# Performance work log

Hardware: AMD Instinct MI355X
Metric: run time of the kernel (lower is better)

Reference implementation:

```python
import jax, jax.numpy as jnp
from jax import lax
import numpy as np

DIM = 256
RANK = 128
E = 4      # num_experts
K = 2      # top_k
B, H, W = 8, 128, 128


def setup_inputs() -> dict:
    key = jax.random.key(0)
    ks = jax.random.split(key, 12)
    s = lambda fan: 1.0 / np.sqrt(fan)
    return {
        "x": jax.random.normal(ks[0], (B, DIM, H, W), jnp.float32),
        "shared": jax.random.normal(ks[1], (B, DIM, H, W), jnp.float32),
        # FrequencyEmbedding MLP (torch Linear: weight [out,in], bias [out])
        "mlp_w1": jax.random.normal(ks[2], (2 * DIM, DIM), jnp.float32) * s(DIM),
        "mlp_b1": jnp.zeros((2 * DIM,), jnp.float32),
        "mlp_w2": jax.random.normal(ks[3], (DIM, 2 * DIM), jnp.float32) * s(2 * DIM),
        "mlp_b2": jnp.zeros((DIM,), jnp.float32),
        # routing gates (no bias)
        "gate_w": jax.random.normal(ks[4], (E, DIM), jnp.float32) * s(DIM),
        "freq_gate_w": jax.random.normal(ks[5], (E, DIM), jnp.float32) * s(DIM),
        # stacked expert 1x1 convs: proj0/proj1 dim->rank, proj2 rank->dim
        "p0": jax.random.normal(ks[6], (E, RANK, DIM), jnp.float32) * s(DIM),
        "p1": jax.random.normal(ks[7], (E, RANK, DIM), jnp.float32) * s(DIM),
        "p2": jax.random.normal(ks[8], (E, DIM, RANK), jnp.float32) * s(RANK),
        # output 1x1 conv (no bias)
        "proj_out_w": jax.random.normal(ks[9], (DIM, DIM), jnp.float32) * s(DIM),
    }


def _high_pass_depthwise(x):
    # fixed frozen 3x3 high-pass kernel, depthwise (groups=C)
    C = x.shape[1]
    k = jnp.array([[-1., -1., -1.], [-1., 8., -1.], [-1., -1., -1.]], x.dtype)
    k = jnp.tile(k[None, None], (C, 1, 1, 1))  # [C,1,3,3]
    return lax.conv_general_dilated(
        x, k, window_strides=(1, 1), padding="SAME",
        feature_group_count=C,
        dimension_numbers=("NCHW", "OIHW", "NCHW"))


def reference(x, shared, mlp_w1, mlp_b1, mlp_w2, mlp_b2,
              gate_w, freq_gate_w, p0, p1, p2, proj_out_w):
    Bn = x.shape[0]
    # FrequencyEmbedding: high-pass conv -> GELU -> global mean -> MLP
    h = jax.nn.gelu(_high_pass_depthwise(x), approximate=False)
    h = h.mean(axis=(-2, -1))                                    # [B, C]
    freq_emb = jax.nn.gelu(h @ mlp_w1.T + mlp_b1, approximate=False) @ mlp_w2.T + mlp_b2
    # Routing: avg-pool gate + freq gate, softmax, top-k, scatter to dense gates
    pooled = x.mean(axis=(-2, -1))                               # [B, C]
    logits = pooled @ gate_w.T + freq_emb @ freq_gate_w.T        # [B, E]
    gating = jax.nn.softmax(logits, axis=-1)
    vals, idx = lax.top_k(gating, K)                             # [B, K]
    gates = jnp.zeros_like(logits).at[jnp.arange(Bn)[:, None], idx].set(vals)  # [B, E]
    a = jnp.einsum("erd,bdhw->berhw", p0, x)                     # [B,E,R,H,W]
    b = jnp.einsum("erd,bdhw->berhw", p1, shared)
    y = a * jax.nn.silu(b)
    # gate-weighted combine, folding gates into the contraction; shortcut term
    combined = (jnp.einsum("be,edr,berhw->bdhw", gates, p2, y)
                + gates.sum(-1)[:, None, None, None] * x)        # [B,C,H,W]
    out = jnp.einsum("od,bdhw->bohw", proj_out_w, combined)
    return out
```

## Files before the change

kernel.cpp:

```cpp
#include <hip/hip_runtime.h>
#include <math.h>

#define DIMC 256
#define HW   16384
#define NB   8
#define HID  512
#define NE   4
#define RNK  128

typedef __bf16 bf16x8 __attribute__((ext_vector_type(8)));
typedef float  f32x4  __attribute__((ext_vector_type(4)));
typedef float  f32x16 __attribute__((ext_vector_type(16)));

__device__ __forceinline__ unsigned short f2bf(float f) {
  unsigned u = __builtin_bit_cast(unsigned, f);
  u += 0x7FFFu + ((u >> 16) & 1u);
  return (unsigned short)(u >> 16);
}
__device__ __forceinline__ unsigned pack2(float a, float b) {
  return (unsigned)f2bf(a) | ((unsigned)f2bf(b) << 16);
}
__device__ __forceinline__ float bf2f(unsigned short u) {
  unsigned v = ((unsigned)u) << 16;
  return __builtin_bit_cast(float, v);
}

#define CPAD 136
__global__ __launch_bounds__(256) void k_conv_reduce(const float* __restrict__ x,
                                                     float* __restrict__ xsum,
                                                     float* __restrict__ hsum) {
  __shared__ unsigned short sp[128 * CPAD];
  __shared__ float red[8];
  const int p = blockIdx.x;
  const int tid = threadIdx.x;
  const float4* img4 = (const float4*)(x + (size_t)p * HW);
#pragma unroll
  for (int u = 0; u < 16; ++u) {
    const int unit = tid + 256 * u;
    const float4 v = img4[unit];
    const int row = unit >> 5, xq = unit & 31;
    uint2 w;
    w.x = pack2(v.x, v.y);
    w.y = pack2(v.z, v.w);
    *(uint2*)&sp[row * CPAD + xq * 4] = w;
  }
  __syncthreads();

  float xacc = 0.f, hacc = 0.f;
#pragma unroll
  for (int u = 0; u < 4; ++u) {
    const int seg = tid + 256 * u;
    const int row = seg >> 3, x0 = (seg & 7) * 16;
    float S[16], c[16];
#pragma unroll
    for (int j = 0; j < 16; ++j) S[j] = 0.f;
#pragma unroll
    for (int dr = -1; dr <= 1; ++dr) {
      const int r2 = row + dr;
      float v[18];
      if ((unsigned)r2 <= 127u) {
        const unsigned short* rp = sp + r2 * CPAD + x0;
        const uint4 q0 = *(const uint4*)(rp);
        const uint4 q1 = *(const uint4*)(rp + 8);
        v[0]  = (x0 > 0)        ? bf2f(rp[-1]) : 0.f;
        v[17] = (x0 + 16 < 128) ? bf2f(rp[16]) : 0.f;
        v[1] = bf2f((unsigned short)(q0.x & 0xffff)); v[2] = bf2f((unsigned short)(q0.x >> 16));
        v[3] = bf2f((unsigned short)(q0.y & 0xffff)); v[4] = bf2f((unsigned short)(q0.y >> 16));
        v[5] = bf2f((unsigned short)(q0.z & 0xffff)); v[6] = bf2f((unsigned short)(q0.z >> 16));
        v[7] = bf2f((unsigned short)(q0.w & 0xffff)); v[8] = bf2f((unsigned short)(q0.w >> 16));
        v[9]  = bf2f((unsigned short)(q1.x & 0xffff)); v[10] = bf2f((unsigned short)(q1.x >> 16));
        v[11] = bf2f((unsigned short)(q1.y & 0xffff)); v[12] = bf2f((unsigned short)(q1.y >> 16));
        v[13] = bf2f((unsigned short)(q1.z & 0xffff)); v[14] = bf2f((unsigned short)(q1.z >> 16));
        v[15] = bf2f((unsigned short)(q1.w & 0xffff)); v[16] = bf2f((unsigned short)(q1.w >> 16));
      } else {
#pragma unroll
        for (int j = 0; j < 18; ++j) v[j] = 0.f;
      }
      if (dr == 0) {
#pragma unroll
        for (int j = 0; j < 16; ++j) c[j] = v[j + 1];
      }
#pragma unroll
      for (int j = 0; j < 16; ++j) S[j] += v[j] + v[j + 1] + v[j + 2];
    }
#pragma unroll
    for (int j = 0; j < 16; ++j) {
      const float h = 9.f * c[j] - S[j];
      hacc += 0.5f * h * (1.f + erff(h * 0.70710678118654752f));
      xacc += c[j];
    }
  }
#pragma unroll
  for (int off = 32; off > 0; off >>= 1) {
    xacc += __shfl_down(xacc, off);
    hacc += __shfl_down(hacc, off);
  }
  const int wid = tid >> 6, lane = tid & 63;
  if (lane == 0) { red[wid] = xacc; red[4 + wid] = hacc; }
  __syncthreads();
  if (tid == 0) {
    xsum[p] = red[0] + red[1] + red[2] + red[3];
    hsum[p] = red[4] + red[5] + red[6] + red[7];
  }
}

__global__ __launch_bounds__(256) void k_gate_t1(
    const float* __restrict__ hsum, const float* __restrict__ w1,
    const float* __restrict__ b1, float* __restrict__ t1) {
  const int blk = blockIdx.x;
  const int b = blk >> 7;
  const int o = (blk & 127) * 4 + (threadIdx.x >> 6);
  const int lane = threadIdx.x & 63;
  const float4 h = *(const float4*)(hsum + b * DIMC + lane * 4);
  const float4 w = *(const float4*)(w1 + (size_t)o * DIMC + lane * 4);
  float acc = h.x * w.x + h.y * w.y + h.z * w.z + h.w * w.w;
#pragma unroll
  for (int off = 32; off > 0; off >>= 1) acc += __shfl_down(acc, off);
  if (lane == 0) {
    acc = acc * (1.f / 16384.f) + b1[o];
    t1[b * HID + o] = 0.5f * acc * (1.f + erff(acc * 0.70710678118654752f));
  }
}

__global__ __launch_bounds__(256) void k_gate_fe(
    const float* __restrict__ t1, const float* __restrict__ w2,
    const float* __restrict__ b2, float* __restrict__ fe) {
  const int blk = blockIdx.x;
  const int b = blk >> 6;
  const int o = (blk & 63) * 4 + (threadIdx.x >> 6);
  const int lane = threadIdx.x & 63;
  const float* tr = t1 + b * HID + lane * 8;
  const float* wr = w2 + (size_t)o * HID + lane * 8;
  const float4 ta = *(const float4*)tr,  tb = *(const float4*)(tr + 4);
  const float4 wa = *(const float4*)wr,  wb = *(const float4*)(wr + 4);
  float acc = ta.x * wa.x + ta.y * wa.y + ta.z * wa.z + ta.w * wa.w
            + tb.x * wb.x + tb.y * wb.y + tb.z * wb.z + tb.w * wb.w;
#pragma unroll
  for (int off = 32; off > 0; off >>= 1) acc += __shfl_down(acc, off);
  if (lane == 0) fe[b * DIMC + o] = acc + b2[o];
}

__global__ __launch_bounds__(256) void k_gate_fin(
    const float* __restrict__ xsum, const float* __restrict__ fe,
    const float* __restrict__ gw, const float* __restrict__ fgw,
    float* __restrict__ gates, float* __restrict__ gsumv, int* __restrict__ sel) {
  __shared__ float slog[NB][NE];
  const int wave = threadIdx.x >> 6, lane = threadIdx.x & 63;
  const int e = wave;
  const float4 g1 = *(const float4*)(gw + e * DIMC + lane * 4);
  const float4 g2 = *(const float4*)(fgw + e * DIMC + lane * 4);
  for (int b = 0; b < NB; ++b) {
    const float4 p = *(const float4*)(xsum + b * DIMC + lane * 4);
    const float4 f = *(const float4*)(fe + b * DIMC + lane * 4);
    float acc = (p.x * g1.x + p.y * g1.y + p.z * g1.z + p.w * g1.w) * (1.f / 16384.f)
              + f.x * g2.x + f.y * g2.y + f.z * g2.z + f.w * g2.w;
#pragma unroll
    for (int off = 32; off > 0; off >>= 1) acc += __shfl_down(acc, off);
    if (lane == 0) slog[b][e] = acc;
  }
  __syncthreads();
  if (threadIdx.x < NB) {
    const int b = threadIdx.x;
    float l[4] = {slog[b][0], slog[b][1], slog[b][2], slog[b][3]};
    const float m = fmaxf(fmaxf(l[0], l[1]), fmaxf(l[2], l[3]));
    float g[4];
    float ssum = 0.f;
    for (int e2 = 0; e2 < 4; ++e2) { g[e2] = expf(l[e2] - m); ssum += g[e2]; }
    for (int e2 = 0; e2 < 4; ++e2) g[e2] /= ssum;
    int i1 = 0;
    for (int e2 = 1; e2 < 4; ++e2) if (g[e2] > g[i1]) i1 = e2;
    int i2 = -1;
    for (int e2 = 0; e2 < 4; ++e2) {
      if (e2 == i1) continue;
      if (i2 < 0 || g[e2] > g[i2]) i2 = e2;
    }
    for (int e2 = 0; e2 < 4; ++e2)
      gates[b * 4 + e2] = (e2 == i1) ? g[i1] : ((e2 == i2) ? g[i2] : 0.f);
    gsumv[b] = g[i1] + g[i2];
    sel[b * 2 + 0] = i1;
    sel[b * 2 + 1] = i2;
  }
}

__global__ __launch_bounds__(128) void k_q2(const float* __restrict__ wp,
                                            const float* __restrict__ p2,
                                            float* __restrict__ q2) {
  const int eo = blockIdx.x;
  const int e = eo >> 8, o = eo & 255;
  const int r = threadIdx.x;
  const float* p2e = p2 + (size_t)e * DIMC * RNK;
  const float* wrow = wp + (size_t)o * DIMC;
  float acc = 0.f;
  for (int d = 0; d < DIMC; ++d) acc += wrow[d] * p2e[d * RNK + r];
  q2[(size_t)eo * RNK + r] = acc;
}

__global__ __launch_bounds__(256) void k_build(
    const float* __restrict__ p0, const float* __restrict__ p1,
    const float* __restrict__ wp, const float* __restrict__ q2,
    const float* __restrict__ gates, const float* __restrict__ gsumv,
    const int* __restrict__ sel,
    unsigned* __restrict__ A1u, unsigned* __restrict__ A2u,
    unsigned* __restrict__ A3u) {
  const int total = NB * 32768;
  for (int id = blockIdx.x * 256 + threadIdx.x; id < total;
       id += gridDim.x * 256) {
    const int b = id >> 15;
    const int gi = id & 32767;
    uint4 wv;
    unsigned* dst;
    if (gi < 16384) {
      const int t = gi >> 13;
      const int gj = gi & 8191;
      const int rowblk = gj >> 10, ks = (gj >> 6) & 15;
      const int h = (gj >> 5) & 1, r = gj & 31;
      const int row = rowblk * 32 + r;
      const int e = sel[b * 2 + (row >> 7)];
      const float* src = (t ? p1 : p0) + ((size_t)e * 128 + (row & 127)) * 256
                       + ks * 16 + h * 8;
      const float4 v0 = *(const float4*)src;
      const float4 v1 = *(const float4*)(src + 4);
      wv.x = pack2(v0.x, v0.y); wv.y = pack2(v0.z, v0.w);
      wv.z = pack2(v1.x, v1.y); wv.w = pack2(v1.z, v1.w);
      dst = (t ? A2u : A1u) + (size_t)b * 32768 + gj * 4;
    } else {
      const int gj = gi - 16384;
      const int rowblk = gj >> 11, ks = (gj >> 6) & 31;
      const int h = (gj >> 5) & 1, r = gj & 31;
      const int o = rowblk * 32 + r;
      const int k = ks * 16 + h * 8;
      float v[8];
      if (k < 256) {
        const int e = sel[b * 2 + (k >> 7)];
        const float gsc = gates[b * 4 + e];
        const float* qq = q2 + ((size_t)e * 256 + o) * RNK + (k & 127);
#pragma unroll
        for (int j = 0; j < 8; ++j) v[j] = gsc * qq[j];
      } else {
        const float gs = gsumv[b];
        const float* wr = wp + (size_t)o * DIMC + (k - 256);
#pragma unroll
        for (int j = 0; j < 8; ++j) v[j] = gs * wr[j];
      }
      wv.x = pack2(v[0], v[1]); wv.y = pack2(v[2], v[3]);
      wv.z = pack2(v[4], v[5]); wv.w = pack2(v[6], v[7]);
      dst = A3u + (size_t)b * 65536 + gj * 4;
    }
    *(uint4*)dst = wv;
  }
}

__global__ __launch_bounds__(512, 4) void k_main_mfma(
    const float* __restrict__ x, const float* __restrict__ shr,
    const unsigned short* __restrict__ A1b, const unsigned short* __restrict__ A2b,
    const unsigned short* __restrict__ A3b, float* __restrict__ out) {
  __shared__ unsigned short XF[16384];
  __shared__ unsigned short SF[16384];
  const int tid = threadIdx.x;
  const int b = blockIdx.x & 7;
  const int tile = blockIdx.x >> 3;
  const int nb0 = tile * 64;
  const int wave = tid >> 6;
  const int lane = tid & 63;
  const int r32 = lane & 31;
  const int h = lane >> 5;
  const int wrow = wave * 32;
  const size_t pbase = (size_t)b * DIMC * HW + nb0;

  {
    const int px = lane;
#pragma unroll
    for (int pass = 0; pass < 4; ++pass) {
      const int dblk = pass * 8 + wave;
      const float* xc = x   + pbase + (size_t)(dblk * 8) * HW + px;
      const float* sc = shr + pbase + (size_t)(dblk * 8) * HW + px;
      float vx[8], vs[8];
#pragma unroll
      for (int jj = 0; jj < 8; ++jj) {
        vx[jj] = xc[(size_t)jj * HW];
        vs[jj] = sc[(size_t)jj * HW];
      }
      const int o = dblk * 512 + ((px ^ (dblk & 7)) << 3);
      uint4 wv;
      wv.x = pack2(vx[0], vx[1]); wv.y = pack2(vx[2], vx[3]);
      wv.z = pack2(vx[4], vx[5]); wv.w = pack2(vx[6], vx[7]);
      *(uint4*)&XF[o] = wv;
      uint4 sv;
      sv.x = pack2(vs[0], vs[1]); sv.y = pack2(vs[2], vs[3]);
      sv.z = pack2(vs[4], vs[5]); sv.w = pack2(vs[6], vs[7]);
      *(uint4*)&SF[o] = sv;
    }
  }
  __syncthreads();

  const unsigned short* A1w = A1b + (size_t)(b * 8 + wave) * 8192;
  const unsigned short* A2w = A2b + (size_t)(b * 8 + wave) * 8192;
  const unsigned short* A3w = A3b + (size_t)(b * 8 + wave) * 16384;

  f32x16 accB0 = (f32x16)0.f, accB1 = (f32x16)0.f;
#pragma unroll
  for (int ks = 0; ks < 16; ++ks) {
    const bf16x8 a = *(const bf16x8*)(A2w + ks * 512 + lane * 8);
    const int dblkB = ks * 2 + h;
    const int eb = dblkB * 512 + ((r32 ^ (dblkB & 7)) << 3);
    const bf16x8 b0 = *(const bf16x8*)&SF[eb];
    const bf16x8 b1 = *(const bf16x8*)&SF[eb + 256];
    accB0 = __builtin_amdgcn_mfma_f32_32x32x16_bf16(a, b0, accB0, 0, 0, 0);
    accB1 = __builtin_amdgcn_mfma_f32_32x32x16_bf16(a, b1, accB1, 0, 0, 0);
  }

  f32x16 accA0 = (f32x16)0.f, accA1 = (f32x16)0.f;
#pragma unroll
  for (int ks = 0; ks < 16; ++ks) {
    const bf16x8 a1 = *(const bf16x8*)(A1w + ks * 512 + lane * 8);
    const int dblkB = ks * 2 + h;
    const int eb = dblkB * 512 + ((r32 ^ (dblkB & 7)) << 3);
    const bf16x8 b0 = *(const bf16x8*)&XF[eb];
    const bf16x8 b1 = *(const bf16x8*)&XF[eb + 256];
    accA0 = __builtin_amdgcn_mfma_f32_32x32x16_bf16(a1, b0, accA0, 0, 0, 0);
    accA1 = __builtin_amdgcn_mfma_f32_32x32x16_bf16(a1, b1, accA1, 0, 0, 0);
  }
  __syncthreads();

#pragma unroll
  for (int q = 0; q < 4; ++q) {
    const int dblk = wave * 4 + q;
    const int sw = dblk & 7;
    const int base = dblk * 512 + h * 4;
    float y0[4], y1[4];
#pragma unroll
    for (int i = 0; i < 4; ++i) {
      const float bA = accB0[q * 4 + i];
      const float bBv = accB1[q * 4 + i];
      y0[i] = accA0[q * 4 + i] * (bA / (1.f + __expf(-bA)));
      y1[i] = accA1[q * 4 + i] * (bBv / (1.f + __expf(-bBv)));
    }
    uint2 w0; w0.x = pack2(y0[0], y0[1]); w0.y = pack2(y0[2], y0[3]);
    *(uint2*)&SF[base + ((r32 ^ sw) << 3)] = w0;
    uint2 w1; w1.x = pack2(y1[0], y1[1]); w1.y = pack2(y1[2], y1[3]);
    *(uint2*)&SF[base + (((32 + r32) ^ sw) << 3)] = w1;
  }
  __syncthreads();

  f32x16 accO0 = (f32x16)0.f, accO1 = (f32x16)0.f;
#pragma unroll
  for (int ks = 0; ks < 32; ++ks) {
    const bf16x8 a3 = *(const bf16x8*)(A3w + ks * 512 + lane * 8);
    const int kk = ks & 15;
    const unsigned short* Bsrc = (ks < 16) ? SF : XF;
    const int dblkB = kk * 2 + h;
    const int eb = dblkB * 512 + ((r32 ^ (dblkB & 7)) << 3);
    const bf16x8 b0 = *(const bf16x8*)&Bsrc[eb];
    const bf16x8 b1 = *(const bf16x8*)&Bsrc[eb + 256];
    accO0 = __builtin_amdgcn_mfma_f32_32x32x16_bf16(a3, b0, accO0, 0, 0, 0);
    accO1 = __builtin_amdgcn_mfma_f32_32x32x16_bf16(a3, b1, accO1, 0, 0, 0);
  }

  {
    float* ob = out + pbase;
#pragma unroll
    for (int r = 0; r < 16; ++r) {
      const int row = wrow + (r & 3) + 8 * (r >> 2) + 4 * h;
      ob[(size_t)row * HW + r32] = accO0[r];
      ob[(size_t)row * HW + 32 + r32] = accO1[r];
    }
  }
}

extern "C" void kernel_launch(void* const* d_in, const int* in_sizes, int n_in,
                              void* d_out, int out_size, void* d_ws, size_t ws_size,
                              hipStream_t stream) {
  (void)in_sizes; (void)n_in; (void)out_size; (void)ws_size;
  const float* x   = (const float*)d_in[0];
  const float* shr = (const float*)d_in[1];
  const float* w1  = (const float*)d_in[2];
  const float* b1  = (const float*)d_in[3];
  const float* w2  = (const float*)d_in[4];
  const float* b2  = (const float*)d_in[5];
  const float* gw  = (const float*)d_in[6];
  const float* fgw = (const float*)d_in[7];
  const float* p0  = (const float*)d_in[8];
  const float* p1  = (const float*)d_in[9];
  const float* p2  = (const float*)d_in[10];
  const float* wp  = (const float*)d_in[11];
  float* out = (float*)d_out;

  float* ws    = (float*)d_ws;
  float* xsum  = ws;
  float* hsum  = ws + 2048;
  float* gates = ws + 4096;
  float* gsumv = ws + 4128;
  int*   sel   = (int*)(ws + 4136);
  float* q2    = ws + 4152;
  unsigned* A1u = (unsigned*)(ws + 135224);
  unsigned* A2u = A1u + NB * 256 * 128;
  unsigned* A3u = A2u + NB * 256 * 128;
  float* t1g   = (float*)(A3u + NB * 256 * 256);
  float* feg   = t1g + NB * HID;

  k_conv_reduce<<<NB * DIMC, 256, 0, stream>>>(x, xsum, hsum);
  k_gate_t1<<<1024, 256, 0, stream>>>(hsum, w1, b1, t1g);
  k_gate_fe<<<512, 256, 0, stream>>>(t1g, w2, b2, feg);
  k_gate_fin<<<1, 256, 0, stream>>>(xsum, feg, gw, fgw, gates, gsumv, sel);
  k_q2<<<NE * DIMC, 128, 0, stream>>>(wp, p2, q2);
  k_build<<<512, 256, 0, stream>>>(p0, p1, wp, q2, gates, gsumv, sel, A1u, A2u, A3u);
  k_main_mfma<<<2048, 512, 0, stream>>>(x, shr,
      (const unsigned short*)A1u, (const unsigned short*)A2u,
      (const unsigned short*)A3u, out);
}
```

Baseline: 264.4 us.

## Fuse gating MLP kernels into one per-batch kernel, retile q2, use native bf16 casts

Merges the three gating kernels (t1, freq embedding, final softmax/top-k) into one kernel with one block per batch, keeping intermediates in shared memory and removing two launches plus global round trips. Rewrites k_q2 so each block stages 32 rows of proj_out_w in LDS and each thread accumulates 16 outputs, cutting redundant global loads. Replaces the manual bit-twiddling float-to-bf16 packing with native __bf16 conversions, which may lower to hardware convert instructions. The fused gating kernel runs on only 8 blocks, so its dot products are long serial loops with little parallelism.

Result: slower. 342.1 us (+29.4%).

```diff
diff --git a/kernel.cpp b/kernel.cpp
--- a/kernel.cpp
+++ b/kernel.cpp
@@ -9,17 +9,10 @@
 #define RNK  128
 
 typedef __bf16 bf16x8 __attribute__((ext_vector_type(8)));
+typedef __bf16 bf16x4 __attribute__((ext_vector_type(4)));
 typedef float  f32x4  __attribute__((ext_vector_type(4)));
 typedef float  f32x16 __attribute__((ext_vector_type(16)));
 
-__device__ __forceinline__ unsigned short f2bf(float f) {
-  unsigned u = __builtin_bit_cast(unsigned, f);
-  u += 0x7FFFu + ((u >> 16) & 1u);
-  return (unsigned short)(u >> 16);
-}
-__device__ __forceinline__ unsigned pack2(float a, float b) {
-  return (unsigned)f2bf(a) | ((unsigned)f2bf(b) << 16);
-}
 __device__ __forceinline__ float bf2f(unsigned short u) {
   unsigned v = ((unsigned)u) << 16;
   return __builtin_bit_cast(float, v);
@@ -39,10 +32,10 @@
     const int unit = tid + 256 * u;
     const float4 v = img4[unit];
     const int row = unit >> 5, xq = unit & 31;
-    uint2 w;
-    w.x = pack2(v.x, v.y);
-    w.y = pack2(v.z, v.w);
-    *(uint2*)&sp[row * CPAD + xq * 4] = w;
+    bf16x4 w;
+    w[0] = (__bf16)v.x; w[1] = (__bf16)v.y;
+    w[2] = (__bf16)v.z; w[3] = (__bf16)v.w;
+    *(bf16x4*)&sp[row * CPAD + xq * 4] = w;
   }
   __syncthreads();
 
@@ -104,64 +97,59 @@
   }
 }
 
-__global__ __launch_bounds__(256) void k_gate_t1(
-    const float* __restrict__ hsum, const float* __restrict__ w1,
-    const float* __restrict__ b1, float* __restrict__ t1) {
-  const int blk = blockIdx.x;
-  const int b = blk >> 7;
-  const int o = (blk & 127) * 4 + (threadIdx.x >> 6);
-  const int lane = threadIdx.x & 63;
-  const float4 h = *(const float4*)(hsum + b * DIMC + lane * 4);
-  const float4 w = *(const float4*)(w1 + (size_t)o * DIMC + lane * 4);
-  float acc = h.x * w.x + h.y * w.y + h.z * w.z + h.w * w.w;
-#pragma unroll
-  for (int off = 32; off > 0; off >>= 1) acc += __shfl_down(acc, off);
-  if (lane == 0) {
-    acc = acc * (1.f / 16384.f) + b1[o];
-    t1[b * HID + o] = 0.5f * acc * (1.f + erff(acc * 0.70710678118654752f));
-  }
-}
-
-__global__ __launch_bounds__(256) void k_gate_fe(
-    const float* __restrict__ t1, const float* __restrict__ w2,
-    const float* __restrict__ b2, float* __restrict__ fe) {
-  const int blk = blockIdx.x;
-  const int b = blk >> 6;
-  const int o = (blk & 63) * 4 + (threadIdx.x >> 6);
-  const int lane = threadIdx.x & 63;
-  const float* tr = t1 + b * HID + lane * 8;
-  const float* wr = w2 + (size_t)o * HID + lane * 8;
-  const float4 ta = *(const float4*)tr,  tb = *(const float4*)(tr + 4);
-  const float4 wa = *(const float4*)wr,  wb = *(const float4*)(wr + 4);
-  float acc = ta.x * wa.x + ta.y * wa.y + ta.z * wa.z + ta.w * wa.w
-            + tb.x * wb.x + tb.y * wb.y + tb.z * wb.z + tb.w * wb.w;
-#pragma unroll
-  for (int off = 32; off > 0; off >>= 1) acc += __shfl_down(acc, off);
-  if (lane == 0) fe[b * DIMC + o] = acc + b2[o];
-}
-
-__global__ __launch_bounds__(256) void k_gate_fin(
-    const float* __restrict__ xsum, const float* __restrict__ fe,
+__global__ __launch_bounds__(256) void k_gate_all(
+    const float* __restrict__ xsum, const float* __restrict__ hsum,
+    const float* __restrict__ w1, const float* __restrict__ b1,
+    const float* __restrict__ w2, const float* __restrict__ b2,
     const float* __restrict__ gw, const float* __restrict__ fgw,
     float* __restrict__ gates, float* __restrict__ gsumv, int* __restrict__ sel) {
-  __shared__ float slog[NB][NE];
-  const int wave = threadIdx.x >> 6, lane = threadIdx.x & 63;
-  const int e = wave;
-  const float4 g1 = *(const float4*)(gw + e * DIMC + lane * 4);
-  const float4 g2 = *(const float4*)(fgw + e * DIMC + lane * 4);
-  for (int b = 0; b < NB; ++b) {
-    const float4 p = *(const float4*)(xsum + b * DIMC + lane * 4);
-    const float4 f = *(const float4*)(fe + b * DIMC + lane * 4);
-    float acc = (p.x * g1.x + p.y * g1.y + p.z * g1.z + p.w * g1.w) * (1.f / 16384.f)
+  __shared__ float sh[DIMC], spool[DIMC], st1[HID], sfe[DIMC], slog[NE];
+  const int b = blockIdx.x;
+  const int tid = threadIdx.x;
+  sh[tid]    = hsum[b * DIMC + tid] * (1.f / 16384.f);
+  spool[tid] = xsum[b * DIMC + tid] * (1.f / 16384.f);
+  __syncthreads();
+#pragma unroll
+  for (int oo = 0; oo < 2; ++oo) {
+    const int o = tid + oo * 256;
+    const float* wr = w1 + (size_t)o * DIMC;
+    float acc = b1[o];
+#pragma unroll 8
+    for (int d = 0; d < DIMC; d += 4) {
+      const float4 w = *(const float4*)(wr + d);
+      const float4 h = *(const float4*)(&sh[d]);
+      acc += h.x * w.x + h.y * w.y + h.z * w.z + h.w * w.w;
+    }
+    st1[o] = 0.5f * acc * (1.f + erff(acc * 0.70710678118654752f));
+  }
+  __syncthreads();
+  {
+    const float* wr = w2 + (size_t)tid * HID;
+    float acc = b2[tid];
+#pragma unroll 8
+    for (int d = 0; d < HID; d += 4) {
+      const float4 w = *(const float4*)(wr + d);
+      const float4 h = *(const float4*)(&st1[d]);
+      acc += h.x * w.x + h.y * w.y + h.z * w.z + h.w * w.w;
+    }
+    sfe[tid] = acc;
+  }
+  __syncthreads();
+  {
+    const int wv = tid >> 6, lane = tid & 63;
+    const float4 g1 = *(const float4*)(gw + wv * DIMC + lane * 4);
+    const float4 g2 = *(const float4*)(fgw + wv * DIMC + lane * 4);
+    const float4 p = *(const float4*)(&spool[lane * 4]);
+    const float4 f = *(const float4*)(&sfe[lane * 4]);
+    float acc = p.x * g1.x + p.y * g1.y + p.z * g1.z + p.w * g1.w
               + f.x * g2.x + f.y * g2.y + f.z * g2.z + f.w * g2.w;
 #pragma unroll
     for (int off = 32; off > 0; off >>= 1) acc += __shfl_down(acc, off);
-    if (lane == 0) slog[b][e] = acc;
-  }
-  __syncthreads();
-  if (threadIdx.x < NB) {
-    const int b = threadIdx.x;
-    float l[4] = {slog[b][0], slog[b][1], slog[b][2], slog[b][3]};
+    if (lane == 0) slog[wv] = acc;
+  }
+  __syncthreads();
+  if (tid == 0) {
+    float l[4] = {slog[0], slog[1], slog[2], slog[3]};
     const float m = fmaxf(fmaxf(l[0], l[1]), fmaxf(l[2], l[3]));
     float g[4];
     float ssum = 0.f;
@@ -182,17 +170,40 @@
   }
 }
 
-__global__ __launch_bounds__(128) void k_q2(const float* __restrict__ wp,
+__global__ __launch_bounds__(256) void k_q2(const float* __restrict__ wp,
                                             const float* __restrict__ p2,
                                             float* __restrict__ q2) {
-  const int eo = blockIdx.x;
-  const int e = eo >> 8, o = eo & 255;
-  const int r = threadIdx.x;
-  const float* p2e = p2 + (size_t)e * DIMC * RNK;
-  const float* wrow = wp + (size_t)o * DIMC;
-  float acc = 0.f;
-  for (int d = 0; d < DIMC; ++d) acc += wrow[d] * p2e[d * RNK + r];
-  q2[(size_t)eo * RNK + r] = acc;
+  __shared__ float sw[DIMC * 32];
+  const int e = blockIdx.x >> 3;
+  const int og = blockIdx.x & 7;
+  const int tid = threadIdx.x;
+  const int r = tid & 127;
+  const int half = tid >> 7;
+  for (int i = tid; i < 32 * DIMC; i += 256) {
+    const int ol = i & 31, d = i >> 5;
+    sw[d * 32 + ol] = wp[(size_t)(og * 32 + ol) * DIMC + d];
+  }
+  __syncthreads();
+  const float* p2e = p2 + (size_t)e * DIMC * RNK + r;
+  float acc[16];
+#pragma unroll
+  for (int i = 0; i < 16; ++i) acc[i] = 0.f;
+#pragma unroll 4
+  for (int d = 0; d < DIMC; ++d) {
+    const float pv = p2e[(size_t)d * RNK];
+    const float4* wrow = (const float4*)&sw[d * 32 + half * 16];
+#pragma unroll
+    for (int q = 0; q < 4; ++q) {
+      const float4 w4 = wrow[q];
+      acc[q * 4 + 0] += w4.x * pv;
+      acc[q * 4 + 1] += w4.y * pv;
+      acc[q * 4 + 2] += w4.z * pv;
+      acc[q * 4 + 3] += w4.w * pv;
+    }
+  }
+#pragma unroll
+  for (int i = 0; i < 16; ++i)
+    q2[((size_t)e * 256 + og * 32 + half * 16 + i) * RNK + r] = acc[i];
 }
 
 __global__ __launch_bounds__(256) void k_build(
@@ -207,7 +218,7 @@
        id += gridDim.x * 256) {
     const int b = id >> 15;
     const int gi = id & 32767;
-    uint4 wv;
+    bf16x8 gvec;
     unsigned* dst;
     if (gi < 16384) {
       const int t = gi >> 13;
@@ -220,8 +231,10 @@
                        + ks * 16 + h * 8;
       const float4 v0 = *(const float4*)src;
       const float4 v1 = *(const float4*)(src + 4);
-      wv.x = pack2(v0.x, v0.y); wv.y = pack2(v0.z, v0.w);
-      wv.z = pack2(v1.x, v1.y); wv.w = pack2(v1.z, v1.w);
+      gvec[0] = (__bf16)v0.x; gvec[1] = (__bf16)v0.y;
+      gvec[2] = (__bf16)v0.z; gvec[3] = (__bf16)v0.w;
+      gvec[4] = (__bf16)v1.x; gvec[5] = (__bf16)v1.y;
+      gvec[6] = (__bf16)v1.z; gvec[7] = (__bf16)v1.w;
       dst = (t ? A2u : A1u) + (size_t)b * 32768 + gj * 4;
     } else {
       const int gj = gi - 16384;
@@ -242,11 +255,11 @@
 #pragma unroll
         for (int j = 0; j < 8; ++j) v[j] = gs * wr[j];
       }
-      wv.x = pack2(v[0], v[1]); wv.y = pack2(v[2], v[3]);
-      wv.z = pack2(v[4], v[5]); wv.w = pack2(v[6], v[7]);
+#pragma unroll
+      for (int j = 0; j < 8; ++j) gvec[j] = (__bf16)v[j];
       dst = A3u + (size_t)b * 65536 + gj * 4;
     }
-    *(uint4*)dst = wv;
+    *(bf16x8*)dst = gvec;
   }
 }
 
@@ -281,14 +294,14 @@
         vs[jj] = sc[(size_t)jj * HW];
       }
       const int o = dblk * 512 + ((px ^ (dblk & 7)) << 3);
-      uint4 wv;
-      wv.x = pack2(vx[0], vx[1]); wv.y = pack2(vx[2], vx[3]);
-      wv.z = pack2(vx[4], vx[5]); wv.w = pack2(vx[6], vx[7]);
-      *(uint4*)&XF[o] = wv;
-      uint4 sv;
-      sv.x = pack2(vs[0], vs[1]); sv.y = pack2(vs[2], vs[3]);
-      sv.z = pack2(vs[4], vs[5]); sv.w = pack2(vs[6], vs[7]);
-      *(uint4*)&SF[o] = sv;
+      bf16x8 wv, sv;
+#pragma unroll
+      for (int jj = 0; jj < 8; ++jj) {
+        wv[jj] = (__bf16)vx[jj];
+        sv[jj] = (__bf16)vs[jj];
+      }
+      *(bf16x8*)&XF[o] = wv;
+      *(bf16x8*)&SF[o] = sv;
     }
   }
   __syncthreads();
@@ -335,10 +348,14 @@
       y0[i] = accA0[q * 4 + i] * (bA / (1.f + __expf(-bA)));
       y1[i] = accA1[q * 4 + i] * (bBv / (1.f + __expf(-bBv)));
     }
-    uint2 w0; w0.x = pack2(y0[0], y0[1]); w0.y = pack2(y0[2], y0[3]);
-    *(uint2*)&SF[base + ((r32 ^ sw) << 3)] = w0;
-    uint2 w1; w1.x = pack2(y1[0], y1[1]); w1.y = pack2(y1[2], y1[3]);
-    *(uint2*)&SF[base + (((32 + r32) ^ sw) << 3)] = w1;
+    bf16x4 w0, w1v;
+#pragma unroll
+    for (int i = 0; i < 4; ++i) {
+      w0[i]  = (__bf16)y0[i];
+      w1v[i] = (__bf16)y1[i];
+    }
+    *(bf16x4*)&SF[base + ((r32 ^ sw) << 3)] = w0;
+    *(bf16x4*)&SF[base + (((32 + r32) ^ sw) << 3)] = w1v;
   }
   __syncthreads();
 
@@ -395,14 +412,11 @@
   unsigned* A1u = (unsigned*)(ws + 135224);
   unsigned* A2u = A1u + NB * 256 * 128;
   unsigned* A3u = A2u + NB * 256 * 128;
-  float* t1g   = (float*)(A3u + NB * 256 * 256);
-  float* feg   = t1g + NB * HID;
 
   k_conv_reduce<<<NB * DIMC, 256, 0, stream>>>(x, xsum, hsum);
-  k_gate_t1<<<1024, 256, 0, stream>>>(hsum, w1, b1, t1g);
-  k_gate_fe<<<512, 256, 0, stream>>>(t1g, w2, b2, feg);
-  k_gate_fin<<<1, 256, 0, stream>>>(xsum, feg, gw, fgw, gates, gsumv, sel);
-  k_q2<<<NE * DIMC, 128, 0, stream>>>(wp, p2, q2);
+  k_gate_all<<<NB, 256, 0, stream>>>(xsum, hsum, w1, b1, w2, b2, gw, fgw,
+                                     gates, gsumv, sel);
+  k_q2<<<32, 256, 0, stream>>>(wp, p2, q2);
   k_build<<<512, 256, 0, stream>>>(p0, p1, wp, q2, gates, gsumv, sel, A1u, A2u, A3u);
   k_main_mfma<<<2048, 512, 0, stream>>>(x, shr,
       (const unsigned short*)A1u, (const unsigned short*)A2u,
```
